# Optimization experiments

Hardware: AMD Instinct MI355X
Metric: run time of the kernel (lower is better)

The kernel has to match this reference:

```python
import jax, jax.numpy as jnp
import numpy as np

# Forest of B perfect binary trees, depth D levels, M = 2**D - 1 nodes/tree.
B, D, H, X, VOCAB, NCLS = 32, 12, 256, 256, 32000, 20
M = 2 ** D - 1          # 4095 nodes per tree
N = B * M               # 131040 total nodes


def setup_inputs() -> dict:
    key = jax.random.key(0)
    ks = jax.random.split(key, 9)
    x = jax.random.randint(ks[0], (N,), 0, VOCAB, dtype=jnp.int32)
    # leaves are the last level of each tree: in-tree index >= 2**(D-1)-1
    leaf = (jnp.arange(M) >= 2 ** (D - 1) - 1).astype(jnp.int32)
    x_mask = jnp.tile(leaf, B)  # [N] int32, 1 on leaves, 0 on internal nodes
    s = 0.02
    Emb = jax.random.normal(ks[1], (VOCAB, X), jnp.float32) * s
    W_iou = jax.random.normal(ks[2], (3 * H, X), jnp.float32) * s
    b_iou = jnp.zeros((3 * H,), jnp.float32)
    U_iou = jax.random.normal(ks[3], (3 * H, H), jnp.float32) * s
    U_f = jax.random.normal(ks[4], (H, H), jnp.float32) * s
    b_f = jnp.ones((H,), jnp.float32)  # forget-gate bias init
    W_out = jax.random.normal(ks[5], (NCLS, H), jnp.float32) * s
    b_out = jnp.zeros((NCLS,), jnp.float32)
    return {"x": x, "x_mask": x_mask, "Emb": Emb, "W_iou": W_iou,
            "b_iou": b_iou, "U_iou": U_iou, "U_f": U_f, "b_f": b_f,
            "W_out": W_out, "b_out": b_out}


def reference(x, x_mask, Emb, W_iou, b_iou, U_iou, U_f, b_f, W_out, b_out):
    # input_module: embedding applied to masked ids, result masked again
    x_emb = Emb[x * x_mask] * x_mask[:, None].astype(Emb.dtype)      # [N, X]
    xiou = (x_emb @ W_iou.T).reshape(B, M, 3 * H)                    # W_iou * x per node
    h_sum = jnp.zeros((B, M, H), Emb.dtype)    # sum of children h (childsum)
    fc_sum = jnp.zeros((B, M, H), Emb.dtype)   # sum_k f_k * c_k from children
    h_all = jnp.zeros((B, M, H), Emb.dtype)
    # topological propagation: leaves (deepest level) -> roots
    for l in range(D - 1, -1, -1):
        s_, e_ = 2 ** l - 1, 2 ** (l + 1) - 1  # static in-tree level slice
        iou = xiou[:, s_:e_] + h_sum[:, s_:e_] @ U_iou.T + b_iou
        i, o, u = jnp.split(iou, 3, axis=-1)
        c = jax.nn.sigmoid(i) * jnp.tanh(u) + fc_sum[:, s_:e_]
        h = jax.nn.sigmoid(o) * jnp.tanh(c)
        h_all = h_all.at[:, s_:e_].set(h)
        if l > 0:
            f = jax.nn.sigmoid(h @ U_f.T + b_f)          # per-child forget gate
            parents = (np.arange(s_, e_) - 1) // 2       # static parent indices
            h_sum = h_sum.at[:, parents].add(h)
            fc_sum = fc_sum.at[:, parents].add(f * c)
    # output_module applied to all node states
    return h_all.reshape(N, H) @ W_out.T + b_out                    # [N, NCLS]
```

## Files before the change

kernel.cpp:

```cpp
#include <hip/hip_runtime.h>

#define B_TREES 32
#define DEPTH   12
#define M_NODES 4095
#define N_NODES (B_TREES * M_NODES)
#define HDIM    256
#define VOCAB   32000
#define NCLS    20
#define LEAFROWS 65536
#define LDSH_S 20

typedef _Float16 f16;
typedef _Float16 f16x8 __attribute__((ext_vector_type(8)));
typedef _Float16 f16x4 __attribute__((ext_vector_type(4)));
typedef _Float16 f16x2 __attribute__((ext_vector_type(2)));
typedef float    f32x4 __attribute__((ext_vector_type(4)));

__device__ __forceinline__ float sigf(float x)      { return 1.0f / (1.0f + __expf(-x)); }
__device__ __forceinline__ float tanh_fast(float x) { return 1.0f - 2.0f / (1.0f + __expf(2.0f * x)); }

__global__ __launch_bounds__(256) void cvt_kernel(
    const float4* __restrict__ Emb,  const float4* __restrict__ Wiou,
    const float4* __restrict__ Uiou, const float4* __restrict__ Uf,
    const float4* __restrict__ Wout,
    f16x4* __restrict__ Emb16,  f16x4* __restrict__ Wiou16,
    f16x4* __restrict__ Uiou16, f16x4* __restrict__ Uf16,
    f16x4* __restrict__ Wout16)
{
    int i = blockIdx.x * 256 + threadIdx.x;
    if (i < VOCAB * HDIM / 4) {
        float4 v = Emb[i];
        f16x4 r; r[0] = (f16)v.x; r[1] = (f16)v.y; r[2] = (f16)v.z; r[3] = (f16)v.w;
        Emb16[i] = r;
    }
    if (i < 768 * HDIM / 4) {
        float4 v = Wiou[i];
        f16x4 r; r[0] = (f16)v.x; r[1] = (f16)v.y; r[2] = (f16)v.z; r[3] = (f16)v.w;
        Wiou16[i] = r;
        float4 u = Uiou[i];
        f16x4 s; s[0] = (f16)u.x; s[1] = (f16)u.y; s[2] = (f16)u.z; s[3] = (f16)u.w;
        Uiou16[i] = s;
    }
    if (i < HDIM * HDIM / 4) {
        float4 v = Uf[i];
        f16x4 r; r[0] = (f16)v.x; r[1] = (f16)v.y; r[2] = (f16)v.z; r[3] = (f16)v.w;
        Uf16[i] = r;
    }
    if (i < 32 * HDIM / 4) {
        int row = i >> 6;
        f16x4 r = {};
        if (row < NCLS) {
            float4 v = Wout[i];
            r[0] = (f16)v.x; r[1] = (f16)v.y; r[2] = (f16)v.z; r[3] = (f16)v.w;
        }
        Wout16[i] = r;
    }
}

#define LEAF_TPW 8
__global__ __launch_bounds__(256) void leaf_kernel(
    const int* __restrict__ x, const f16* __restrict__ Emb16,
    const f16* __restrict__ Wiou16, const float* __restrict__ b_iou,
    f16* __restrict__ h16, f16* __restrict__ cT)
{
    __shared__ f16 wlds[1536 * 8];
    __shared__ f16 ldsh[4][16 * LDSH_S];

    const int tid  = threadIdx.x;
    const int lane = tid & 63;
    const int w    = tid >> 6;
    const int quad = lane >> 4;
    const int l15  = lane & 15;
    const int qk   = quad * 8;
    const int cb0  = blockIdx.y * 16;

    #pragma unroll
    for (int i = 0; i < 6; ++i) {
        int f = i * 256 + tid;
        int mat = f >> 9, r = f & 511, ks = r >> 6, q = (r >> 4) & 3, c = r & 15;
        *(f16x8*)(wlds + f * 8) = *(const f16x8*)(Wiou16 +
            (mat * 256 + cb0 + c) * HDIM + ks * 32 + q * 8);
    }
    __syncthreads();

    const float bi = b_iou[cb0 + l15];
    const float bo = b_iou[256 + cb0 + l15];
    const float bu = b_iou[512 + cb0 + l15];

    const int row0 = (blockIdx.x * 4 + w) * (LEAF_TPW * 16);

    int nodeRow = (row0 >> 11) * M_NODES + 2047 + (row0 & 2047);
    int embBase = x[nodeRow + l15] * HDIM;
    f16x8 a[8];
    #pragma unroll
    for (int ks = 0; ks < 8; ++ks)
        a[ks] = *(const f16x8*)(Emb16 + embBase + ks * 32 + qk);

    for (int rt = 0; rt < LEAF_TPW; ++rt) {
        const int rw = row0 + rt * 16;
        const int curNode = nodeRow;
        f16x8 ac[8];
        #pragma unroll
        for (int ks = 0; ks < 8; ++ks) ac[ks] = a[ks];

        if (rt + 1 < LEAF_TPW) {
            const int rwn = rw + 16;
            nodeRow = (rwn >> 11) * M_NODES + 2047 + (rwn & 2047);
            embBase = x[nodeRow + l15] * HDIM;
            #pragma unroll
            for (int ks = 0; ks < 8; ++ks)
                a[ks] = *(const f16x8*)(Emb16 + embBase + ks * 32 + qk);
        }

        f32x4 acc[3] = {};
        #pragma unroll
        for (int ks = 0; ks < 8; ++ks) {
            #pragma unroll
            for (int mat = 0; mat < 3; ++mat) {
                f16x8 wf = *(const f16x8*)(wlds +
                    ((mat * 8 + ks) * 64 + quad * 16 + l15) * 8);
                acc[mat] = __builtin_amdgcn_mfma_f32_16x16x32_f16(
                    ac[ks], wf, acc[mat], 0, 0, 0);
            }
        }

        f16x4 cv;
        #pragma unroll
        for (int r = 0; r < 4; ++r) {
            float i_ = acc[0][r] + bi;
            float o_ = acc[1][r] + bo;
            float u_ = acc[2][r] + bu;
            float c  = sigf(i_) * tanh_fast(u_);
            float h  = sigf(o_) * tanh_fast(c);
            cv[r] = (f16)c;
            ldsh[w][(quad * 4 + r) * LDSH_S + l15] = (f16)h;
        }
        *(f16x4*)(cT + (cb0 + l15) * LEAFROWS + rw + quad * 4) = cv;

        {
            int row_l = lane >> 2, cpos = (lane & 3) * 4;
            f16x4 v = *(const f16x4*)(&ldsh[w][row_l * LDSH_S + cpos]);
            *(f16x4*)(h16 + (curNode + row_l) * HDIM + cb0 + cpos) = v;
        }
    }
}

__global__ __launch_bounds__(256) void fused_level_kernel(
    const f16* __restrict__ Uiou16, const f16* __restrict__ Uf16,
    const float* __restrict__ b_iou, const float* __restrict__ b_f,
    f16* __restrict__ h16, const f16* __restrict__ cT_child,
    f16* __restrict__ cT_parent, int l, int rows_p, int tpw)
{
    __shared__ f16 wlds[2048 * 8];
    __shared__ f16 ldsh[4][16 * LDSH_S];

    const int tid  = threadIdx.x;
    const int lane = tid & 63;
    const int w    = tid >> 6;
    const int quad = lane >> 4;
    const int l15  = lane & 15;
    const int qk   = quad * 8;
    const int cb0  = blockIdx.y * 16;

    #pragma unroll
    for (int i = 0; i < 8; ++i) {
        int f = i * 256 + tid;
        int mat = f >> 9, r = f & 511, ks = r >> 6, q = (r >> 4) & 3, c = r & 15;
        const f16* src = (mat == 0)
            ? (Uf16 + (cb0 + c) * HDIM + ks * 32 + q * 8)
            : (Uiou16 + ((mat - 1) * 256 + cb0 + c) * HDIM + ks * 32 + q * 8);
        *(f16x8*)(wlds + f * 8) = *(const f16x8*)src;
    }
    __syncthreads();

    const float bi  = b_iou[cb0 + l15];
    const float bo  = b_iou[256 + cb0 + l15];
    const float bu  = b_iou[512 + cb0 + l15];
    const float bfv = b_f[cb0 + l15];
    const int lc = l + 1;
    const int maskc = (1 << lc) - 1;
    const int maskp = (1 << l) - 1;
    const int rows_c = rows_p * 2;

    const int p0 = blockIdx.x * (tpw * 64);

    for (int pt = 0; pt < tpw; ++pt) {
        const int pw = p0 + (pt * 4 + w) * 16;
        if (pw >= rows_p) continue;
        const int cw = 2 * pw;

        int childBase0, childBase1;
        {
            int cl0 = cw + l15;
            childBase0 = ((cl0 >> lc) * M_NODES + maskc + (cl0 & maskc)) * HDIM;
            int cl1 = cw + 16 + l15;
            childBase1 = ((cl1 >> lc) * M_NODES + maskc + (cl1 & maskc)) * HDIM;
        }

        f32x4 accf0 = {}, accf1 = {};
        f32x4 au0[3] = {}, au1[3] = {};
        #pragma unroll
        for (int ks = 0; ks < 8; ++ks) {
            const int k0 = ks * 32 + qk;
            f16x8 a0 = *(const f16x8*)(h16 + childBase0 + k0);
            f16x8 a1 = *(const f16x8*)(h16 + childBase1 + k0);
            f16x8 wfF = *(const f16x8*)(wlds + (ks * 64 + quad * 16 + l15) * 8);
            accf0 = __builtin_amdgcn_mfma_f32_16x16x32_f16(a0, wfF, accf0, 0, 0, 0);
            accf1 = __builtin_amdgcn_mfma_f32_16x16x32_f16(a1, wfF, accf1, 0, 0, 0);
            #pragma unroll
            for (int m = 0; m < 3; ++m) {
                f16x8 wm = *(const f16x8*)(wlds +
                    (((m + 1) * 8 + ks) * 64 + quad * 16 + l15) * 8);
                au0[m] = __builtin_amdgcn_mfma_f32_16x16x32_f16(a0, wm, au0[m], 0, 0, 0);
                au1[m] = __builtin_amdgcn_mfma_f32_16x16x32_f16(a1, wm, au1[m], 0, 0, 0);
            }
        }

        #pragma unroll
        for (int s = 0; s < 2; ++s) {
            const f32x4& af = s ? accf1 : accf0;
            const f32x4* au = s ? au1 : au0;
            const int csr = cw + s * 16;
            f16x4 cc = *(const f16x4*)(cT_child +
                (cb0 + l15) * rows_c + csr + quad * 4);
            f16x2 cpack;
            #pragma unroll
            for (int pr = 0; pr < 2; ++pr) {
                float f0 = sigf(af[2 * pr]     + bfv);
                float f1 = sigf(af[2 * pr + 1] + bfv);
                float fc = f0 * (float)cc[2 * pr] + f1 * (float)cc[2 * pr + 1];
                float i_ = au[0][2 * pr] + au[0][2 * pr + 1] + bi;
                float o_ = au[1][2 * pr] + au[1][2 * pr + 1] + bo;
                float u_ = au[2][2 * pr] + au[2][2 * pr + 1] + bu;
                float c  = sigf(i_) * tanh_fast(u_) + fc;
                float h  = sigf(o_) * tanh_fast(c);
                cpack[pr] = (f16)c;
                ldsh[w][(s * 8 + quad * 2 + pr) * LDSH_S + l15] = (f16)h;
            }
            *(f16x2*)(cT_parent + (cb0 + l15) * rows_p + pw + s * 8 + quad * 2) = cpack;
        }

        {
            int prow = lane >> 2, cpos = (lane & 3) * 4;
            int p = pw + prow;
            int b = p >> l, tt = p & maskp;
            int node = b * M_NODES + (1 << l) - 1 + tt;
            f16x4 v = *(const f16x4*)(&ldsh[w][prow * LDSH_S + cpos]);
            *(f16x4*)(h16 + node * HDIM + cb0 + cpos) = v;
        }
    }
}

__global__ __launch_bounds__(256) void out_kernel(
    const f16* __restrict__ h16, const f16* __restrict__ Wout16,
    const float* __restrict__ bout, float* __restrict__ out)
{
    const int lane = threadIdx.x & 63;
    const int w    = threadIdx.x >> 6;
    const int quad = lane >> 4;
    const int l15  = lane & 15;
    const int qk   = quad * 8;

    f16x8 wfk[2][8];
    #pragma unroll
    for (int cf = 0; cf < 2; ++cf)
        #pragma unroll
        for (int ks = 0; ks < 8; ++ks)
            wfk[cf][ks] = *(const f16x8*)(Wout16 +
                (cf * 16 + l15) * HDIM + ks * 32 + qk);
    float bo[2];
    #pragma unroll
    for (int cf = 0; cf < 2; ++cf) {
        int col = cf * 16 + l15;
        bo[cf] = bout[col < NCLS ? col : 0];
    }

    const int tile0  = blockIdx.x * 16;
    const int ntotal = N_NODES / 16;
    const int tend   = (tile0 + 16 < ntotal) ? 16 : (ntotal - tile0);

    for (int rt = w; rt < tend; rt += 4) {
        const int rw = (tile0 + rt) * 16;
        f32x4 acc[2] = {};
        #pragma unroll
        for (int ks = 0; ks < 8; ++ks) {
            f16x8 a = *(const f16x8*)(h16 + (rw + l15) * HDIM + ks * 32 + qk);
            #pragma unroll
            for (int cf = 0; cf < 2; ++cf)
                acc[cf] = __builtin_amdgcn_mfma_f32_16x16x32_f16(
                    a, wfk[cf][ks], acc[cf], 0, 0, 0);
        }
        #pragma unroll
        for (int cf = 0; cf < 2; ++cf) {
            const int col = cf * 16 + l15;
            if (col < NCLS) {
                #pragma unroll
                for (int r = 0; r < 4; ++r)
                    out[(rw + quad * 4 + r) * NCLS + col] = acc[cf][r] + bo[cf];
            }
        }
    }
}

extern "C" void kernel_launch(void* const* d_in, const int* in_sizes, int n_in,
                              void* d_out, int out_size, void* d_ws, size_t ws_size,
                              hipStream_t stream)
{
    const int*   x     = (const int*)d_in[0];
    const float* Emb   = (const float*)d_in[2];
    const float* W_iou = (const float*)d_in[3];
    const float* b_iou = (const float*)d_in[4];
    const float* U_iou = (const float*)d_in[5];
    const float* U_f   = (const float*)d_in[6];
    const float* b_f   = (const float*)d_in[7];
    const float* W_out = (const float*)d_in[8];
    const float* b_out = (const float*)d_in[9];
    float* out = (float*)d_out;

    char* ws = (char*)d_ws;
    size_t off = 0;
    auto take = [&](size_t bytes) -> char* {
        char* p = ws + off; off += (bytes + 255) & ~(size_t)255; return p;
    };
    f16* h16    = (f16*)take((size_t)N_NODES * HDIM * 2);
    f16* cA     = (f16*)take((size_t)HDIM * LEAFROWS * 2);
    f16* cB     = (f16*)take((size_t)HDIM * (LEAFROWS / 2) * 2);
    f16* Emb16  = (f16*)take((size_t)VOCAB * HDIM * 2);
    f16* Wiou16 = (f16*)take((size_t)768 * HDIM * 2);
    f16* Uiou16 = (f16*)take((size_t)768 * HDIM * 2);
    f16* Uf16   = (f16*)take((size_t)HDIM * HDIM * 2);
    f16* Wout16 = (f16*)take((size_t)32 * HDIM * 2);

    cvt_kernel<<<VOCAB * HDIM / 4 / 256, 256, 0, stream>>>(
        (const float4*)Emb, (const float4*)W_iou, (const float4*)U_iou,
        (const float4*)U_f, (const float4*)W_out,
        (f16x4*)Emb16, (f16x4*)Wiou16, (f16x4*)Uiou16, (f16x4*)Uf16,
        (f16x4*)Wout16);

    leaf_kernel<<<dim3(LEAFROWS / (4 * 16 * LEAF_TPW), 16), 256, 0, stream>>>(
        x, Emb16, Wiou16, b_iou, h16, cA);

    f16* cin  = cA;
    f16* cout_ = cB;
    for (int l = 10; l >= 0; --l) {
        int rows_p = B_TREES << l;
        int tpw = rows_p / (64 * 128); if (tpw < 1) tpw = 1;
        int gx  = (rows_p + tpw * 64 - 1) / (tpw * 64);
        fused_level_kernel<<<dim3(gx, 16), 256, 0, stream>>>(
            Uiou16, Uf16, b_iou, b_f, h16, cin, cout_, l, rows_p, tpw);
        f16* t = cin; cin = cout_; cout_ = t;
    }

    out_kernel<<<dim3((N_NODES / 16 + 15) / 16), 256, 0, stream>>>(
        h16, Wout16, b_out, out);
}
```

Measured before the change: 410.4 us.

## Software-pipeline child h loads in level and output kernels, halve per-iteration tile

The fused level kernel now processes 8-parent (16-child) sets per iteration instead of 16-parent tiles, and prefetches the next set's child h fragments and child c values into registers while MFMAs run on the current set. The grid sizing changes to spread sets over more waves. The output kernel gives each wave four contiguous tiles and prefetches the next tile's h rows in the same way. This targets global load latency on these memory-bound kernels. The cost is more registers, smaller h stores, and fewer MFMAs per loaded weight fragment.

```diff
diff --git a/kernel.cpp b/kernel.cpp
--- a/kernel.cpp
+++ b/kernel.cpp
@@ -149,10 +149,10 @@
     const f16* __restrict__ Uiou16, const f16* __restrict__ Uf16,
     const float* __restrict__ b_iou, const float* __restrict__ b_f,
     f16* __restrict__ h16, const f16* __restrict__ cT_child,
-    f16* __restrict__ cT_parent, int l, int rows_p, int tpw)
+    f16* __restrict__ cT_parent, int l, int rows_p, int spw)
 {
     __shared__ f16 wlds[2048 * 8];
-    __shared__ f16 ldsh[4][16 * LDSH_S];
+    __shared__ f16 ldsh[4][8 * LDSH_S];
 
     const int tid  = threadIdx.x;
     const int lane = tid & 63;
@@ -181,72 +181,78 @@
     const int maskc = (1 << lc) - 1;
     const int maskp = (1 << l) - 1;
     const int rows_c = rows_p * 2;
-
-    const int p0 = blockIdx.x * (tpw * 64);
-
-    for (int pt = 0; pt < tpw; ++pt) {
-        const int pw = p0 + (pt * 4 + w) * 16;
-        if (pw >= rows_p) continue;
-        const int cw = 2 * pw;
-
-        int childBase0, childBase1;
+    const int sets   = rows_p >> 3;
+
+    const int s0    = (blockIdx.x * 4 + w) * spw;
+    const int nsets = (s0 >= sets) ? 0 : ((sets - s0 < spw) ? sets - s0 : spw);
+    if (nsets <= 0) return;
+
+    f16x8 a[8];
+    f16x4 cc;
+    {
+        int cl = s0 * 16 + l15;
+        int cb = ((cl >> lc) * M_NODES + maskc + (cl & maskc)) * HDIM;
+        #pragma unroll
+        for (int ks = 0; ks < 8; ++ks)
+            a[ks] = *(const f16x8*)(h16 + cb + ks * 32 + qk);
+        cc = *(const f16x4*)(cT_child + (cb0 + l15) * rows_c + s0 * 16 + quad * 4);
+    }
+
+    for (int i = 0; i < nsets; ++i) {
+        const int s = s0 + i;
+        f16x8 ac[8];
+        #pragma unroll
+        for (int ks = 0; ks < 8; ++ks) ac[ks] = a[ks];
+        const f16x4 ccc = cc;
+
         {
-            int cl0 = cw + l15;
-            childBase0 = ((cl0 >> lc) * M_NODES + maskc + (cl0 & maskc)) * HDIM;
-            int cl1 = cw + 16 + l15;
-            childBase1 = ((cl1 >> lc) * M_NODES + maskc + (cl1 & maskc)) * HDIM;
-        }
-
-        f32x4 accf0 = {}, accf1 = {};
-        f32x4 au0[3] = {}, au1[3] = {};
+            const int sn = (i + 1 < nsets) ? s + 1 : s;
+            int cl = sn * 16 + l15;
+            int cb = ((cl >> lc) * M_NODES + maskc + (cl & maskc)) * HDIM;
+            #pragma unroll
+            for (int ks = 0; ks < 8; ++ks)
+                a[ks] = *(const f16x8*)(h16 + cb + ks * 32 + qk);
+            cc = *(const f16x4*)(cT_child + (cb0 + l15) * rows_c + sn * 16 + quad * 4);
+        }
+
+        f32x4 accf = {};
+        f32x4 au[3] = {};
         #pragma unroll
         for (int ks = 0; ks < 8; ++ks) {
-            const int k0 = ks * 32 + qk;
-            f16x8 a0 = *(const f16x8*)(h16 + childBase0 + k0);
-            f16x8 a1 = *(const f16x8*)(h16 + childBase1 + k0);
             f16x8 wfF = *(const f16x8*)(wlds + (ks * 64 + quad * 16 + l15) * 8);
-            accf0 = __builtin_amdgcn_mfma_f32_16x16x32_f16(a0, wfF, accf0, 0, 0, 0);
-            accf1 = __builtin_amdgcn_mfma_f32_16x16x32_f16(a1, wfF, accf1, 0, 0, 0);
+            accf = __builtin_amdgcn_mfma_f32_16x16x32_f16(ac[ks], wfF, accf, 0, 0, 0);
             #pragma unroll
             for (int m = 0; m < 3; ++m) {
                 f16x8 wm = *(const f16x8*)(wlds +
                     (((m + 1) * 8 + ks) * 64 + quad * 16 + l15) * 8);
-                au0[m] = __builtin_amdgcn_mfma_f32_16x16x32_f16(a0, wm, au0[m], 0, 0, 0);
-                au1[m] = __builtin_amdgcn_mfma_f32_16x16x32_f16(a1, wm, au1[m], 0, 0, 0);
+                au[m] = __builtin_amdgcn_mfma_f32_16x16x32_f16(ac[ks], wm, au[m], 0, 0, 0);
             }
         }
 
-        #pragma unroll
-        for (int s = 0; s < 2; ++s) {
-            const f32x4& af = s ? accf1 : accf0;
-            const f32x4* au = s ? au1 : au0;
-            const int csr = cw + s * 16;
-            f16x4 cc = *(const f16x4*)(cT_child +
-                (cb0 + l15) * rows_c + csr + quad * 4);
-            f16x2 cpack;
-            #pragma unroll
-            for (int pr = 0; pr < 2; ++pr) {
-                float f0 = sigf(af[2 * pr]     + bfv);
-                float f1 = sigf(af[2 * pr + 1] + bfv);
-                float fc = f0 * (float)cc[2 * pr] + f1 * (float)cc[2 * pr + 1];
-                float i_ = au[0][2 * pr] + au[0][2 * pr + 1] + bi;
-                float o_ = au[1][2 * pr] + au[1][2 * pr + 1] + bo;
-                float u_ = au[2][2 * pr] + au[2][2 * pr + 1] + bu;
-                float c  = sigf(i_) * tanh_fast(u_) + fc;
-                float h  = sigf(o_) * tanh_fast(c);
-                cpack[pr] = (f16)c;
-                ldsh[w][(s * 8 + quad * 2 + pr) * LDSH_S + l15] = (f16)h;
-            }
-            *(f16x2*)(cT_parent + (cb0 + l15) * rows_p + pw + s * 8 + quad * 2) = cpack;
-        }
+        const int pw8 = s * 8;
+        f16x2 cpack;
+        #pragma unroll
+        for (int pr = 0; pr < 2; ++pr) {
+            float f0 = sigf(accf[2 * pr]     + bfv);
+            float f1 = sigf(accf[2 * pr + 1] + bfv);
+            float fc = f0 * (float)ccc[2 * pr] + f1 * (float)ccc[2 * pr + 1];
+            float i_ = au[0][2 * pr] + au[0][2 * pr + 1] + bi;
+            float o_ = au[1][2 * pr] + au[1][2 * pr + 1] + bo;
+            float u_ = au[2][2 * pr] + au[2][2 * pr + 1] + bu;
+            float c  = sigf(i_) * tanh_fast(u_) + fc;
+            float h  = sigf(o_) * tanh_fast(c);
+            cpack[pr] = (f16)c;
+            ldsh[w][(quad * 2 + pr) * LDSH_S + l15] = (f16)h;
+        }
+        *(f16x2*)(cT_parent + (cb0 + l15) * rows_p + pw8 + quad * 2) = cpack;
 
         {
-            int prow = lane >> 2, cpos = (lane & 3) * 4;
-            int p = pw + prow;
+            int prow = lane >> 3, cpos = (lane & 7) * 2;
+            int p = pw8 + prow;
             int b = p >> l, tt = p & maskp;
             int node = b * M_NODES + (1 << l) - 1 + tt;
-            f16x4 v = *(const f16x4*)(&ldsh[w][prow * LDSH_S + cpos]);
-            *(f16x4*)(h16 + node * HDIM + cb0 + cpos) = v;
+            f16x2 v = *(const f16x2*)(&ldsh[w][prow * LDSH_S + cpos]);
+            *(f16x2*)(h16 + node * HDIM + cb0 + cpos) = v;
         }
     }
 }
@@ -275,21 +281,37 @@
         bo[cf] = bout[col < NCLS ? col : 0];
     }
 
-    const int tile0  = blockIdx.x * 16;
     const int ntotal = N_NODES / 16;
-    const int tend   = (tile0 + 16 < ntotal) ? 16 : (ntotal - tile0);
-
-    for (int rt = w; rt < tend; rt += 4) {
-        const int rw = (tile0 + rt) * 16;
+    const int t0     = blockIdx.x * 16 + w * 4;
+    const int tn     = (t0 >= ntotal) ? 0 : ((ntotal - t0 < 4) ? ntotal - t0 : 4);
+    if (tn <= 0) return;
+
+    f16x8 a[8];
+    #pragma unroll
+    for (int ks = 0; ks < 8; ++ks)
+        a[ks] = *(const f16x8*)(h16 + (t0 * 16 + l15) * HDIM + ks * 32 + qk);
+
+    for (int i = 0; i < tn; ++i) {
+        const int rw = (t0 + i) * 16;
+        f16x8 ac[8];
+        #pragma unroll
+        for (int ks = 0; ks < 8; ++ks) ac[ks] = a[ks];
+
+        {
+            const int tnx = (i + 1 < tn) ? t0 + i + 1 : t0 + i;
+            #pragma unroll
+            for (int ks = 0; ks < 8; ++ks)
+                a[ks] = *(const f16x8*)(h16 + (tnx * 16 + l15) * HDIM + ks * 32 + qk);
+        }
+
         f32x4 acc[2] = {};
         #pragma unroll
-        for (int ks = 0; ks < 8; ++ks) {
-            f16x8 a = *(const f16x8*)(h16 + (rw + l15) * HDIM + ks * 32 + qk);
+        for (int ks = 0; ks < 8; ++ks)
             #pragma unroll
             for (int cf = 0; cf < 2; ++cf)
                 acc[cf] = __builtin_amdgcn_mfma_f32_16x16x32_f16(
-                    a, wfk[cf][ks], acc[cf], 0, 0, 0);
-        }
+                    ac[ks], wfk[cf][ks], acc[cf], 0, 0, 0);
+
         #pragma unroll
         for (int cf = 0; cf < 2; ++cf) {
             const int col = cf * 16 + l15;
@@ -344,10 +366,11 @@
     f16* cout_ = cB;
     for (int l = 10; l >= 0; --l) {
         int rows_p = B_TREES << l;
-        int tpw = rows_p / (64 * 128); if (tpw < 1) tpw = 1;
-        int gx  = (rows_p + tpw * 64 - 1) / (tpw * 64);
+        int sets   = rows_p >> 3;
+        int spw    = sets / 512; if (spw < 1) spw = 1;
+        int gx     = (sets + 4 * spw - 1) / (4 * spw);
         fused_level_kernel<<<dim3(gx, 16), 256, 0, stream>>>(
-            Uiou16, Uf16, b_iou, b_f, h16, cin, cout_, l, rows_p, tpw);
+            Uiou16, Uf16, b_iou, b_f, h16, cin, cout_, l, rows_p, spw);
         f16* t = cin; cin = cout_; cout_ = t;
     }
 
```

After: 444.2 us. +8.2%, slower.

## Swap grid axes, skip LDS weight staging on small levels, prefetch in output

Applied to the files above, without the earlier changes.

Leaf and level kernels swap their grid axes so the 16 column blocks are adjacent in launch order, which should make blocks that share node rows run together for cache reuse. Level work is redistributed as contiguous tiles per wave. Levels with fewer than 512 tiles skip the LDS weight staging and its barrier, reading U weights straight from global/L2. The output kernel assigns contiguous tiles per wave and register-prefetches the next tile's h rows. The direct global weight reads on small levels may cost more than the staging they replace.

```diff
diff --git a/kernel.cpp b/kernel.cpp
--- a/kernel.cpp
+++ b/kernel.cpp
@@ -72,7 +72,7 @@
     const int quad = lane >> 4;
     const int l15  = lane & 15;
     const int qk   = quad * 8;
-    const int cb0  = blockIdx.y * 16;
+    const int cb0  = blockIdx.x * 16;
 
     #pragma unroll
     for (int i = 0; i < 6; ++i) {
@@ -87,7 +87,7 @@
     const float bo = b_iou[256 + cb0 + l15];
     const float bu = b_iou[512 + cb0 + l15];
 
-    const int row0 = (blockIdx.x * 4 + w) * (LEAF_TPW * 16);
+    const int row0 = (blockIdx.y * 4 + w) * (LEAF_TPW * 16);
 
     int nodeRow = (row0 >> 11) * M_NODES + 2047 + (row0 & 2047);
     int embBase = x[nodeRow + l15] * HDIM;
@@ -145,13 +145,14 @@
     }
 }
 
+template <bool STAGE>
 __global__ __launch_bounds__(256) void fused_level_kernel(
     const f16* __restrict__ Uiou16, const f16* __restrict__ Uf16,
     const float* __restrict__ b_iou, const float* __restrict__ b_f,
     f16* __restrict__ h16, const f16* __restrict__ cT_child,
     f16* __restrict__ cT_parent, int l, int rows_p, int tpw)
 {
-    __shared__ f16 wlds[2048 * 8];
+    __shared__ f16 wlds[STAGE ? 2048 * 8 : 8];
     __shared__ f16 ldsh[4][16 * LDSH_S];
 
     const int tid  = threadIdx.x;
@@ -160,18 +161,20 @@
     const int quad = lane >> 4;
     const int l15  = lane & 15;
     const int qk   = quad * 8;
-    const int cb0  = blockIdx.y * 16;
-
-    #pragma unroll
-    for (int i = 0; i < 8; ++i) {
-        int f = i * 256 + tid;
-        int mat = f >> 9, r = f & 511, ks = r >> 6, q = (r >> 4) & 3, c = r & 15;
-        const f16* src = (mat == 0)
-            ? (Uf16 + (cb0 + c) * HDIM + ks * 32 + q * 8)
-            : (Uiou16 + ((mat - 1) * 256 + cb0 + c) * HDIM + ks * 32 + q * 8);
-        *(f16x8*)(wlds + f * 8) = *(const f16x8*)src;
-    }
-    __syncthreads();
+    const int cb0  = blockIdx.x * 16;
+
+    if (STAGE) {
+        #pragma unroll
+        for (int i = 0; i < 8; ++i) {
+            int f = i * 256 + tid;
+            int mat = f >> 9, r = f & 511, ks = r >> 6, q = (r >> 4) & 3, c = r & 15;
+            const f16* src = (mat == 0)
+                ? (Uf16 + (cb0 + c) * HDIM + ks * 32 + q * 8)
+                : (Uiou16 + ((mat - 1) * 256 + cb0 + c) * HDIM + ks * 32 + q * 8);
+            *(f16x8*)(wlds + f * 8) = *(const f16x8*)src;
+        }
+        __syncthreads();
+    }
 
     const float bi  = b_iou[cb0 + l15];
     const float bo  = b_iou[256 + cb0 + l15];
@@ -181,12 +184,13 @@
     const int maskc = (1 << lc) - 1;
     const int maskp = (1 << l) - 1;
     const int rows_c = rows_p * 2;
-
-    const int p0 = blockIdx.x * (tpw * 64);
-
-    for (int pt = 0; pt < tpw; ++pt) {
-        const int pw = p0 + (pt * 4 + w) * 16;
-        if (pw >= rows_p) continue;
+    const int tiles  = rows_p >> 4;
+
+    const int t0 = (blockIdx.y * 4 + w) * tpw;
+    const int nt = (t0 >= tiles) ? 0 : ((tiles - t0 < tpw) ? tiles - t0 : tpw);
+
+    for (int i = 0; i < nt; ++i) {
+        const int pw = (t0 + i) * 16;
         const int cw = 2 * pw;
 
         int childBase0, childBase1;
@@ -204,13 +208,16 @@
             const int k0 = ks * 32 + qk;
             f16x8 a0 = *(const f16x8*)(h16 + childBase0 + k0);
             f16x8 a1 = *(const f16x8*)(h16 + childBase1 + k0);
-            f16x8 wfF = *(const f16x8*)(wlds + (ks * 64 + quad * 16 + l15) * 8);
+            f16x8 wfF = STAGE
+                ? *(const f16x8*)(wlds + (ks * 64 + quad * 16 + l15) * 8)
+                : *(const f16x8*)(Uf16 + (cb0 + l15) * HDIM + k0);
             accf0 = __builtin_amdgcn_mfma_f32_16x16x32_f16(a0, wfF, accf0, 0, 0, 0);
             accf1 = __builtin_amdgcn_mfma_f32_16x16x32_f16(a1, wfF, accf1, 0, 0, 0);
             #pragma unroll
             for (int m = 0; m < 3; ++m) {
-                f16x8 wm = *(const f16x8*)(wlds +
-                    (((m + 1) * 8 + ks) * 64 + quad * 16 + l15) * 8);
+                f16x8 wm = STAGE
+                    ? *(const f16x8*)(wlds + (((m + 1) * 8 + ks) * 64 + quad * 16 + l15) * 8)
+                    : *(const f16x8*)(Uiou16 + (m * 256 + cb0 + l15) * HDIM + k0);
                 au0[m] = __builtin_amdgcn_mfma_f32_16x16x32_f16(a0, wm, au0[m], 0, 0, 0);
                 au1[m] = __builtin_amdgcn_mfma_f32_16x16x32_f16(a1, wm, au1[m], 0, 0, 0);
             }
@@ -275,21 +282,37 @@
         bo[cf] = bout[col < NCLS ? col : 0];
     }
 
-    const int tile0  = blockIdx.x * 16;
     const int ntotal = N_NODES / 16;
-    const int tend   = (tile0 + 16 < ntotal) ? 16 : (ntotal - tile0);
-
-    for (int rt = w; rt < tend; rt += 4) {
-        const int rw = (tile0 + rt) * 16;
+    const int t0     = blockIdx.x * 16 + w * 4;
+    const int tn     = (t0 >= ntotal) ? 0 : ((ntotal - t0 < 4) ? ntotal - t0 : 4);
+    if (tn <= 0) return;
+
+    f16x8 a[8];
+    #pragma unroll
+    for (int ks = 0; ks < 8; ++ks)
+        a[ks] = *(const f16x8*)(h16 + (t0 * 16 + l15) * HDIM + ks * 32 + qk);
+
+    for (int i = 0; i < tn; ++i) {
+        const int rw = (t0 + i) * 16;
+        f16x8 ac[8];
+        #pragma unroll
+        for (int ks = 0; ks < 8; ++ks) ac[ks] = a[ks];
+
+        {
+            const int tnx = (i + 1 < tn) ? t0 + i + 1 : t0 + i;
+            #pragma unroll
+            for (int ks = 0; ks < 8; ++ks)
+                a[ks] = *(const f16x8*)(h16 + (tnx * 16 + l15) * HDIM + ks * 32 + qk);
+        }
+
         f32x4 acc[2] = {};
         #pragma unroll
-        for (int ks = 0; ks < 8; ++ks) {
-            f16x8 a = *(const f16x8*)(h16 + (rw + l15) * HDIM + ks * 32 + qk);
+        for (int ks = 0; ks < 8; ++ks)
             #pragma unroll
             for (int cf = 0; cf < 2; ++cf)
                 acc[cf] = __builtin_amdgcn_mfma_f32_16x16x32_f16(
-                    a, wfk[cf][ks], acc[cf], 0, 0, 0);
-        }
+                    ac[ks], wfk[cf][ks], acc[cf], 0, 0, 0);
+
         #pragma unroll
         for (int cf = 0; cf < 2; ++cf) {
             const int col = cf * 16 + l15;
@@ -337,17 +360,22 @@
         (f16x4*)Emb16, (f16x4*)Wiou16, (f16x4*)Uiou16, (f16x4*)Uf16,
         (f16x4*)Wout16);
 
-    leaf_kernel<<<dim3(LEAFROWS / (4 * 16 * LEAF_TPW), 16), 256, 0, stream>>>(
+    leaf_kernel<<<dim3(16, LEAFROWS / (4 * 16 * LEAF_TPW)), 256, 0, stream>>>(
         x, Emb16, Wiou16, b_iou, h16, cA);
 
     f16* cin  = cA;
     f16* cout_ = cB;
     for (int l = 10; l >= 0; --l) {
         int rows_p = B_TREES << l;
-        int tpw = rows_p / (64 * 128); if (tpw < 1) tpw = 1;
-        int gx  = (rows_p + tpw * 64 - 1) / (tpw * 64);
-        fused_level_kernel<<<dim3(gx, 16), 256, 0, stream>>>(
-            Uiou16, Uf16, b_iou, b_f, h16, cin, cout_, l, rows_p, tpw);
+        int tiles  = rows_p >> 4;
+        int tpw    = tiles / 256; if (tpw < 1) tpw = 1;
+        int gy     = (tiles + 4 * tpw - 1) / (4 * tpw);
+        if (tiles >= 512)
+            fused_level_kernel<true><<<dim3(16, gy), 256, 0, stream>>>(
+                Uiou16, Uf16, b_iou, b_f, h16, cin, cout_, l, rows_p, tpw);
+        else
+            fused_level_kernel<false><<<dim3(16, gy), 256, 0, stream>>>(
+                Uiou16, Uf16, b_iou, b_f, h16, cin, cout_, l, rows_p, tpw);
         f16* t = cin; cin = cout_; cout_ = t;
     }
 
```

Result: slower. 464.0 us (+13.1%).
